# Kernel tuning notes

Measured on AMD Instinct MI355X. Metric: run time of the kernel, lower is better.

The kernel has to match this reference:

```python
import jax, jax.numpy as jnp
import numpy as np

B, S, D, H = 2, 2048, 1024, 16
HD = D // H  # 64

def _make_freqs():
    # flux-style rotation matrices: [1,1,S,HD//2,2,2]
    theta = 10000.0
    inv = 1.0 / (theta ** (np.arange(0, HD, 2, dtype=np.float32) / HD))  # [HD//2]
    pos = np.arange(S, dtype=np.float32)
    ang = pos[:, None] * inv[None, :]  # [S, HD//2]
    cos, sin = np.cos(ang), np.sin(ang)
    rot = np.stack([np.stack([cos, -sin], -1), np.stack([sin, cos], -1)], -2)  # [S,HD//2,2,2]
    return jnp.asarray(rot[None, None], dtype=jnp.float32)

def setup_inputs() -> dict:
    key = jax.random.key(0)
    ks = jax.random.split(key, 9)
    sc = 1.0 / np.sqrt(D)
    return {
        "x": jax.random.normal(ks[0], (B, S, D), jnp.float32),
        "freqs": _make_freqs(),
        "Wq": jax.random.normal(ks[1], (D, D), jnp.float32) * sc,
        "bq": jax.random.normal(ks[2], (D,), jnp.float32) * 0.01,
        "Wk": jax.random.normal(ks[3], (D, D), jnp.float32) * sc,
        "bk": jax.random.normal(ks[4], (D,), jnp.float32) * 0.01,
        "Wv": jax.random.normal(ks[5], (D, D), jnp.float32) * sc,
        "bv": jax.random.normal(ks[6], (D,), jnp.float32) * 0.01,
        "Wo": jax.random.normal(ks[7], (D, D), jnp.float32) * sc,
        "bo": jax.random.normal(ks[8], (D,), jnp.float32) * 0.01,
    }

def _apply_rope(xq, xk, freqs):
    # xq/xk: [B,H,S,HD]; freqs: [1,1,S,HD//2,2,2]
    def rot(t):
        t_ = t.reshape(*t.shape[:-1], -1, 1, 2)  # [B,H,S,HD//2,1,2]
        out = freqs[..., 0] * t_[..., 0] + freqs[..., 1] * t_[..., 1]  # [B,H,S,HD//2,2]
        return out.reshape(t.shape).astype(t.dtype)
    return rot(xq), rot(xk)

def reference(x, freqs, Wq, bq, Wk, bk, Wv, bv, Wo, bo):
    b, s, _ = x.shape
    # QKV projections (torch Linear: x @ W.T + b)
    q = (x @ Wq.T + bq).reshape(b, s, H, HD).transpose(0, 2, 1, 3)  # [B,H,S,HD]
    k = (x @ Wk.T + bk).reshape(b, s, H, HD).transpose(0, 2, 1, 3)
    v = (x @ Wv.T + bv).reshape(b, s, H, HD).transpose(0, 2, 1, 3)
    q, k = _apply_rope(q, k, freqs)
    # scaled dot product attention, no mask, no dropout
    scale = 1.0 / jnp.sqrt(jnp.asarray(HD, x.dtype))
    scores = jnp.einsum("bhqd,bhkd->bhqk", q, k) * scale
    attn = jax.nn.softmax(scores, axis=-1)
    o = jnp.einsum("bhqk,bhkd->bhqd", attn, v)  # [B,H,S,HD]
    o = o.transpose(0, 2, 1, 3).reshape(b, s, D)
    return o @ Wo.T + bo
```

## Files before the change

kernel.cpp:

```cpp
#include <hip/hip_runtime.h>
#include <cmath>

#define B_ 2
#define S_ 2048
#define D_ 1024
#define H_ 16
#define HD_ 64
#define M_ 4096

typedef __attribute__((ext_vector_type(8))) short short8;
typedef __attribute__((ext_vector_type(4))) short short4v;
typedef __attribute__((ext_vector_type(4))) float f32x4;

__device__ __forceinline__ short f2bf(float x) {
    unsigned u = __builtin_bit_cast(unsigned, x);
    u += 0x7fffu + ((u >> 16) & 1u);
    return (short)(u >> 16);
}

__device__ __forceinline__ void gload_lds16(const short* g, short* l) {
    __builtin_amdgcn_global_load_lds(
        (const __attribute__((address_space(1))) unsigned int*)g,
        (__attribute__((address_space(3))) unsigned int*)l, 16, 0, 0);
}

__global__ __launch_bounds__(256) void cast_all_kernel(
    const float* __restrict__ x,  const float* __restrict__ Wq,
    const float* __restrict__ Wk, const float* __restrict__ Wv,
    const float* __restrict__ Wo,
    short* __restrict__ xb, short* __restrict__ Wqkvb, short* __restrict__ Wob)
{
    const size_t i = (size_t)blockIdx.x * 256 + threadIdx.x;
    const float* src; short* dst; size_t off;
    if (i < 1048576)      { src = x;  dst = xb;              off = i; }
    else if (i < 1310720) { src = Wq; dst = Wqkvb;           off = i - 1048576; }
    else if (i < 1572864) { src = Wk; dst = Wqkvb + 1048576; off = i - 1310720; }
    else if (i < 1835008) { src = Wv; dst = Wqkvb + 2097152; off = i - 1572864; }
    else                  { src = Wo; dst = Wob;             off = i - 1835008; }
    float4 v = ((const float4*)src)[off];
    short4v o = { f2bf(v.x), f2bf(v.y), f2bf(v.z), f2bf(v.w) };
    ((short4v*)dst)[off] = o;
}

template<int MODE, int TM, int TN, int NSUB>
__global__ __launch_bounds__(256) void gemm_chunk(
    const short* __restrict__ A, const short* __restrict__ Bw,
    const float* __restrict__ b0p, const float* __restrict__ b1p, const float* __restrict__ b2p,
    const float* __restrict__ freqs,
    void* __restrict__ out0, void* __restrict__ out1, void* __restrict__ out2)
{
    constexpr int RT = TM / 32, CT = TN / 32;
    __shared__ __align__(16) short As[NSUB*TM*32];
    __shared__ __align__(16) short Bs[NSUB*TN*32];
    const int t = threadIdx.x;
    const int w = t >> 6;
    const int lane = t & 63;
    const int qd = lane >> 4, l = lane & 15;
    const int n0 = blockIdx.x * TN, m0 = blockIdx.y * TM;
    const int wr = (w >> 1) * (TM/2), wc = (w & 1) * (TN/2);
    const int srow = lane >> 2;
    const int scol = (lane & 3) * 8;

    f32x4 acc[RT][CT] = {};

    for (int k0 = 0; k0 < 1024; k0 += NSUB*32) {
        __syncthreads();
        #pragma unroll
        for (int sub = 0; sub < NSUB; ++sub) {
            #pragma unroll
            for (int j = 0; j < TM/64; ++j) {
                const int rr = (j*4 + w) * 16;
                gload_lds16(A + (size_t)(m0 + rr + srow)*1024 + k0 + sub*32 + scol,
                            &As[sub*TM*32 + rr*32]);
            }
            #pragma unroll
            for (int j = 0; j < TN/64; ++j) {
                const int rr = (j*4 + w) * 16;
                gload_lds16(Bw + (size_t)(n0 + rr + srow)*1024 + k0 + sub*32 + scol,
                            &Bs[sub*TN*32 + rr*32]);
            }
        }
        __syncthreads();
        #pragma unroll
        for (int sub = 0; sub < NSUB; ++sub) {
            short8 af[RT], bf[CT];
            #pragma unroll
            for (int rt = 0; rt < RT; ++rt)
                af[rt] = *(const short8*)&As[sub*TM*32 + (wr + rt*16 + l)*32 + qd*8];
            #pragma unroll
            for (int ct = 0; ct < CT; ++ct)
                bf[ct] = *(const short8*)&Bs[sub*TN*32 + (wc + ct*16 + l)*32 + qd*8];
            #pragma unroll
            for (int rt = 0; rt < RT; ++rt)
                #pragma unroll
                for (int ct = 0; ct < CT; ++ct)
                    acc[rt][ct] = __builtin_amdgcn_mfma_f32_16x16x32_bf16(af[rt], bf[ct], acc[rt][ct], 0, 0, 0);
        }
    }

    if (MODE == 0) {
        float* out = (float*)out0;
        #pragma unroll
        for (int rt = 0; rt < RT; ++rt)
            #pragma unroll
            for (int ct = 0; ct < CT; ++ct) {
                const int n = n0 + wc + ct*16 + l;
                const float bias = b0p[n];
                #pragma unroll
                for (int r = 0; r < 4; ++r) {
                    const int m = m0 + wr + rt*16 + qd*4 + r;
                    out[(size_t)m*1024 + n] = acc[rt][ct][r] + bias;
                }
            }
    } else {
        const int sel = n0 >> 10;
        const int nb = n0 & 1023;
        const float* bias = (sel == 0) ? b0p : (sel == 1) ? b1p : b2p;
        if (sel < 2) {
            short* outg = (short*)((sel == 0) ? out0 : out1);
            #pragma unroll
            for (int rt = 0; rt < RT; ++rt)
                #pragma unroll
                for (int ct = 0; ct < CT; ++ct) {
                    const int d = nb + wc + ct*16 + l;
                    const float bsv = bias[d];
                    const int h = d >> 6, hd = d & 63;
                    #pragma unroll
                    for (int r = 0; r < 4; ++r) {
                        const int m = m0 + wr + rt*16 + qd*4 + r;
                        const int bb = m >> 11, s = m & 2047;
                        float val = acc[rt][ct][r] + bsv;
                        float pv = __shfl_xor(val, 1);
                        const float* f = freqs + (size_t)s*128 + (size_t)(hd >> 1)*4;
                        float o = (d & 1) ? (f[2]*pv + f[3]*val) : (f[0]*val + f[1]*pv);
                        outg[((size_t)(bb*16 + h)*2048 + s)*64 + hd] = f2bf(o);
                    }
                }
        } else {
            short* outv = (short*)out2;
            #pragma unroll
            for (int rt = 0; rt < RT; ++rt)
                #pragma unroll
                for (int ct = 0; ct < CT; ++ct) {
                    const int d = nb + wc + ct*16 + l;
                    const float bsv = bias[d];
                    const int h = d >> 6, hd = d & 63;
                    const int m0r = m0 + wr + rt*16 + qd*4;
                    const int bb = m0r >> 11, s0 = m0r & 2047;
                    short4v pk;
                    #pragma unroll
                    for (int r = 0; r < 4; ++r) pk[r] = f2bf(acc[rt][ct][r] + bsv);
                    *(short4v*)&outv[((size_t)(bb*16 + h)*64 + hd)*2048 + s0] = pk;
                }
        }
    }
}

__global__ __launch_bounds__(512) void attn_mfma(
    const short* __restrict__ qg, const short* __restrict__ kg,
    const short* __restrict__ vtg, short* __restrict__ og)
{
    __shared__ __align__(16) short Kb[2][64*64];
    __shared__ __align__(16) short Vb[2][64*64];
    __shared__ __align__(16) short Pb[128*64];

    const int t = threadIdx.x;
    const int w = t >> 6;
    const int lane = t & 63;
    const int qd = lane >> 4, l = lane & 15;
    const int l7 = lane & 7;
    const int q0 = blockIdx.x * 128;
    const int bh = blockIdx.y;

    const int rl  = lane >> 3;
    const int ss8 = ((lane & 7) ^ rl) << 3;

    short8 qf[2];
    const short* qb = qg + ((size_t)bh*2048 + q0 + w*16)*64;
    #pragma unroll
    for (int kf = 0; kf < 2; ++kf)
        qf[kf] = *(const short8*)&qb[l*64 + kf*32 + qd*8];

    f32x4 oacc[4] = {};
    float lsum = 0.f;

    const short* kbase = kg  + (size_t)bh*2048*64;
    const short* vbase = vtg + (size_t)bh*64*2048;
    const float SC = 0.125f * 1.44269504088896340736f;

    gload_lds16(kbase + (size_t)(w*8 + rl)*64 + ss8,   &Kb[0][(w*8)*64]);
    gload_lds16(vbase + (size_t)(w*8 + rl)*2048 + ss8, &Vb[0][(w*8)*64]);
    __syncthreads();

    for (int kt = 0; kt < 32; ++kt) {
        const int buf = kt & 1;

        if (kt + 1 < 32) {
            gload_lds16(kbase + (size_t)((kt+1)*64 + w*8 + rl)*64 + ss8,
                        &Kb[buf^1][(w*8)*64]);
            gload_lds16(vbase + (size_t)(w*8 + rl)*2048 + (kt+1)*64 + ss8,
                        &Vb[buf^1][(w*8)*64]);
        }

        f32x4 sacc[4] = {};
        #pragma unroll
        for (int ct = 0; ct < 4; ++ct) {
            short8 k0f = *(const short8*)&Kb[buf][(ct*16 + l)*64 + (((0 + qd) ^ l7) << 3)];
            short8 k1f = *(const short8*)&Kb[buf][(ct*16 + l)*64 + (((4 + qd) ^ l7) << 3)];
            sacc[ct] = __builtin_amdgcn_mfma_f32_16x16x32_bf16(k0f, qf[0], sacc[ct], 0, 0, 0);
            sacc[ct] = __builtin_amdgcn_mfma_f32_16x16x32_bf16(k1f, qf[1], sacc[ct], 0, 0, 0);
        }

        #pragma unroll
        for (int ct = 0; ct < 4; ++ct) {
            float p0 = exp2f(sacc[ct][0] * SC);
            float p1 = exp2f(sacc[ct][1] * SC);
            float p2 = exp2f(sacc[ct][2] * SC);
            float p3 = exp2f(sacc[ct][3] * SC);
            lsum += (p0 + p1) + (p2 + p3);
            union { unsigned u[2]; short4v s; } cv;
            asm("v_cvt_pk_bf16_f32 %0, %1, %2" : "=v"(cv.u[0]) : "v"(p0), "v"(p1));
            asm("v_cvt_pk_bf16_f32 %0, %1, %2" : "=v"(cv.u[1]) : "v"(p2), "v"(p3));
            *(short4v*)&Pb[(w*16 + l)*64 + (((ct*32 + qd*8) ^ (l7 << 4)) >> 1)] = cv.s;
        }

        #pragma unroll
        for (int kf = 0; kf < 2; ++kf) {
            const int so = ((kf*4 + qd) ^ l7) << 3;
            short8 pa = *(const short8*)&Pb[(w*16 + l)*64 + so];
            #pragma unroll
            for (int ht = 0; ht < 4; ++ht) {
                short8 vb = *(const short8*)&Vb[buf][(ht*16 + l)*64 + so];
                oacc[ht] = __builtin_amdgcn_mfma_f32_16x16x32_bf16(pa, vb, oacc[ht], 0, 0, 0);
            }
        }

        __syncthreads();
    }

    lsum += __shfl_xor(lsum, 16);
    lsum += __shfl_xor(lsum, 32);
    float inv[4];
    #pragma unroll
    for (int r = 0; r < 4; ++r)
        inv[r] = 1.0f / __shfl(lsum, qd*4 + r);

    const int bb = bh >> 4, h = bh & 15;
    #pragma unroll
    for (int ht = 0; ht < 4; ++ht)
        #pragma unroll
        for (int r = 0; r < 4; ++r) {
            const int s = q0 + w*16 + qd*4 + r;
            og[((size_t)bb*2048 + s)*1024 + h*64 + ht*16 + l] =
                f2bf(oacc[ht][r] * inv[r]);
        }
}

extern "C" void kernel_launch(void* const* d_in, const int* in_sizes, int n_in,
                              void* d_out, int out_size, void* d_ws, size_t ws_size,
                              hipStream_t stream)
{
    const float* x  = (const float*)d_in[0];
    const float* fr = (const float*)d_in[1];
    const float* Wq = (const float*)d_in[2];
    const float* bq = (const float*)d_in[3];
    const float* Wk = (const float*)d_in[4];
    const float* bk = (const float*)d_in[5];
    const float* Wv = (const float*)d_in[6];
    const float* bv = (const float*)d_in[7];
    const float* Wo = (const float*)d_in[8];
    const float* bo = (const float*)d_in[9];
    float* out = (float*)d_out;

    short* ws    = (short*)d_ws;
    short* xb    = ws;
    short* Wqkvb = xb    + 4194304;
    short* Wob   = Wqkvb + 3145728;
    short* qg    = Wob   + 1048576;
    short* kg    = qg    + 4194304;
    short* vtg   = kg    + 4194304;
    short* og    = vtg   + 4194304;

    cast_all_kernel<<<8192, 256, 0, stream>>>(x, Wq, Wk, Wv, Wo, xb, Wqkvb, Wob);
    gemm_chunk<1,128,128,2><<<dim3(24, 32), 256, 0, stream>>>(xb, Wqkvb, bq, bk, bv, fr, qg, kg, vtg);
    attn_mfma<<<dim3(16, 32), 512, 0, stream>>>(qg, kg, vtg, og);
    gemm_chunk<0,128,64,2><<<dim3(16, 32), 256, 0, stream>>>(og, Wob, bo, nullptr, nullptr, nullptr,
                                                             out, nullptr, nullptr);
}
```

Measured before the change: 253.6 us.

## Double-buffer GEMM LDS tiles with XOR-swizzled layout to overlap loads

```diff
diff --git a/kernel.cpp b/kernel.cpp
--- a/kernel.cpp
+++ b/kernel.cpp
@@ -42,60 +42,78 @@
     ((short4v*)dst)[off] = o;
 }
 
-template<int MODE, int TM, int TN, int NSUB>
-__global__ __launch_bounds__(256) void gemm_chunk(
+template<int MODE, int TM, int TN>
+__global__ __launch_bounds__(256) void gemm_db(
     const short* __restrict__ A, const short* __restrict__ Bw,
     const float* __restrict__ b0p, const float* __restrict__ b1p, const float* __restrict__ b2p,
     const float* __restrict__ freqs,
     void* __restrict__ out0, void* __restrict__ out1, void* __restrict__ out2)
 {
     constexpr int RT = TM / 32, CT = TN / 32;
-    __shared__ __align__(16) short As[NSUB*TM*32];
-    __shared__ __align__(16) short Bs[NSUB*TN*32];
+    __shared__ __align__(16) short Ab[2][TM*64];
+    __shared__ __align__(16) short Bs[2][TN*64];
     const int t = threadIdx.x;
     const int w = t >> 6;
     const int lane = t & 63;
     const int qd = lane >> 4, l = lane & 15;
+    const int l7 = lane & 7;
     const int n0 = blockIdx.x * TN, m0 = blockIdx.y * TM;
     const int wr = (w >> 1) * (TM/2), wc = (w & 1) * (TN/2);
-    const int srow = lane >> 2;
-    const int scol = (lane & 3) * 8;
+    const int rl  = lane >> 3;
+    const int ss8 = ((lane & 7) ^ rl) << 3;
 
     f32x4 acc[RT][CT] = {};
 
-    for (int k0 = 0; k0 < 1024; k0 += NSUB*32) {
-        __syncthreads();
-        #pragma unroll
-        for (int sub = 0; sub < NSUB; ++sub) {
-            #pragma unroll
-            for (int j = 0; j < TM/64; ++j) {
-                const int rr = (j*4 + w) * 16;
-                gload_lds16(A + (size_t)(m0 + rr + srow)*1024 + k0 + sub*32 + scol,
-                            &As[sub*TM*32 + rr*32]);
-            }
-            #pragma unroll
-            for (int j = 0; j < TN/64; ++j) {
-                const int rr = (j*4 + w) * 16;
-                gload_lds16(Bw + (size_t)(n0 + rr + srow)*1024 + k0 + sub*32 + scol,
-                            &Bs[sub*TN*32 + rr*32]);
-            }
-        }
-        __syncthreads();
-        #pragma unroll
-        for (int sub = 0; sub < NSUB; ++sub) {
-            short8 af[RT], bf[CT];
-            #pragma unroll
-            for (int rt = 0; rt < RT; ++rt)
-                af[rt] = *(const short8*)&As[sub*TM*32 + (wr + rt*16 + l)*32 + qd*8];
-            #pragma unroll
-            for (int ct = 0; ct < CT; ++ct)
-                bf[ct] = *(const short8*)&Bs[sub*TN*32 + (wc + ct*16 + l)*32 + qd*8];
+    #pragma unroll
+    for (int j = 0; j < TM/32; ++j) {
+        const int r0 = (j*4 + w) * 8;
+        gload_lds16(A + (size_t)(m0 + r0 + rl)*1024 + ss8, &Ab[0][r0*64]);
+    }
+    #pragma unroll
+    for (int j = 0; j < TN/32; ++j) {
+        const int r0 = (j*4 + w) * 8;
+        gload_lds16(Bw + (size_t)(n0 + r0 + rl)*1024 + ss8, &Bs[0][r0*64]);
+    }
+    __syncthreads();
+
+    for (int kt = 0; kt < 16; ++kt) {
+        const int buf = kt & 1;
+
+        if (kt + 1 < 16) {
+            const int k0 = (kt + 1) * 64;
+            #pragma unroll
+            for (int j = 0; j < TM/32; ++j) {
+                const int r0 = (j*4 + w) * 8;
+                gload_lds16(A + (size_t)(m0 + r0 + rl)*1024 + k0 + ss8, &Ab[buf^1][r0*64]);
+            }
+            #pragma unroll
+            for (int j = 0; j < TN/32; ++j) {
+                const int r0 = (j*4 + w) * 8;
+                gload_lds16(Bw + (size_t)(n0 + r0 + rl)*1024 + k0 + ss8, &Bs[buf^1][r0*64]);
+            }
+        }
+
+        #pragma unroll
+        for (int sub = 0; sub < 2; ++sub) {
+            short8 af[RT], bfr[CT];
+            #pragma unroll
+            for (int rt = 0; rt < RT; ++rt) {
+                const int R = wr + rt*16 + l;
+                af[rt] = *(const short8*)&Ab[buf][R*64 + (((sub*4 + qd) ^ l7) << 3)];
+            }
+            #pragma unroll
+            for (int ct = 0; ct < CT; ++ct) {
+                const int R = wc + ct*16 + l;
+                bfr[ct] = *(const short8*)&Bs[buf][R*64 + (((sub*4 + qd) ^ l7) << 3)];
+            }
             #pragma unroll
             for (int rt = 0; rt < RT; ++rt)
                 #pragma unroll
                 for (int ct = 0; ct < CT; ++ct)
-                    acc[rt][ct] = __builtin_amdgcn_mfma_f32_16x16x32_bf16(af[rt], bf[ct], acc[rt][ct], 0, 0, 0);
-        }
+                    acc[rt][ct] = __builtin_amdgcn_mfma_f32_16x16x32_bf16(af[rt], bfr[ct], acc[rt][ct], 0, 0, 0);
+        }
+
+        __syncthreads();
     }
 
     if (MODE == 0) {
@@ -282,8 +300,8 @@
     short* og    = vtg   + 4194304;
 
     cast_all_kernel<<<8192, 256, 0, stream>>>(x, Wq, Wk, Wv, Wo, xb, Wqkvb, Wob);
-    gemm_chunk<1,128,128,2><<<dim3(24, 32), 256, 0, stream>>>(xb, Wqkvb, bq, bk, bv, fr, qg, kg, vtg);
+    gemm_db<1,128,128><<<dim3(24, 32), 256, 0, stream>>>(xb, Wqkvb, bq, bk, bv, fr, qg, kg, vtg);
     attn_mfma<<<dim3(16, 32), 512, 0, stream>>>(qg, kg, vtg, og);
-    gemm_chunk<0,128,64,2><<<dim3(16, 32), 256, 0, stream>>>(og, Wob, bo, nullptr, nullptr, nullptr,
-                                                             out, nullptr, nullptr);
-}
+    gemm_db<0,128,64><<<dim3(16, 32), 256, 0, stream>>>(og, Wob, bo, nullptr, nullptr, nullptr,
+                                                        out, nullptr, nullptr);
+}
```

Measured after the change: 259.6 us. 1.02x slower.

## Double-buffer GEMM K-loop with swizzled LDS and unroll attention ping-pong

Applied to the files above, without the earlier changes.

```diff
diff --git a/kernel.cpp b/kernel.cpp
--- a/kernel.cpp
+++ b/kernel.cpp
@@ -42,60 +42,68 @@
     ((short4v*)dst)[off] = o;
 }
 
-template<int MODE, int TM, int TN, int NSUB>
-__global__ __launch_bounds__(256) void gemm_chunk(
+template<int MODE, int TM, int TN>
+__global__ __launch_bounds__(256) void gemm_db(
     const short* __restrict__ A, const short* __restrict__ Bw,
     const float* __restrict__ b0p, const float* __restrict__ b1p, const float* __restrict__ b2p,
     const float* __restrict__ freqs,
     void* __restrict__ out0, void* __restrict__ out1, void* __restrict__ out2)
 {
     constexpr int RT = TM / 32, CT = TN / 32;
-    __shared__ __align__(16) short As[NSUB*TM*32];
-    __shared__ __align__(16) short Bs[NSUB*TN*32];
+    __shared__ __align__(16) short A0[TM*32];
+    __shared__ __align__(16) short A1[TM*32];
+    __shared__ __align__(16) short Bs0[TN*32];
+    __shared__ __align__(16) short Bs1[TN*32];
     const int t = threadIdx.x;
     const int w = t >> 6;
     const int lane = t & 63;
     const int qd = lane >> 4, l = lane & 15;
     const int n0 = blockIdx.x * TN, m0 = blockIdx.y * TM;
     const int wr = (w >> 1) * (TM/2), wc = (w & 1) * (TN/2);
-    const int srow = lane >> 2;
-    const int scol = (lane & 3) * 8;
+    const int srow  = lane >> 2;
+    const int sslot = ((lane & 3) ^ ((lane >> 3) & 3)) * 8;
+    const int rsw = (l >> 1) & 3;
 
     f32x4 acc[RT][CT] = {};
 
-    for (int k0 = 0; k0 < 1024; k0 += NSUB*32) {
-        __syncthreads();
-        #pragma unroll
-        for (int sub = 0; sub < NSUB; ++sub) {
-            #pragma unroll
-            for (int j = 0; j < TM/64; ++j) {
-                const int rr = (j*4 + w) * 16;
-                gload_lds16(A + (size_t)(m0 + rr + srow)*1024 + k0 + sub*32 + scol,
-                            &As[sub*TM*32 + rr*32]);
-            }
-            #pragma unroll
-            for (int j = 0; j < TN/64; ++j) {
-                const int rr = (j*4 + w) * 16;
-                gload_lds16(Bw + (size_t)(n0 + rr + srow)*1024 + k0 + sub*32 + scol,
-                            &Bs[sub*TN*32 + rr*32]);
-            }
-        }
-        __syncthreads();
-        #pragma unroll
-        for (int sub = 0; sub < NSUB; ++sub) {
-            short8 af[RT], bf[CT];
-            #pragma unroll
-            for (int rt = 0; rt < RT; ++rt)
-                af[rt] = *(const short8*)&As[sub*TM*32 + (wr + rt*16 + l)*32 + qd*8];
+    auto STAGE = [&](int k0, short* As, short* Bss) {
+        #pragma unroll
+        for (int j = 0; j < TM/64; ++j) {
+            const int r0 = (j*4 + w) * 16;
+            gload_lds16(A + (size_t)(m0 + r0 + srow)*1024 + k0 + sslot, &As[r0*32]);
+        }
+        #pragma unroll
+        for (int j = 0; j < TN/64; ++j) {
+            const int r0 = (j*4 + w) * 16;
+            gload_lds16(Bw + (size_t)(n0 + r0 + srow)*1024 + k0 + sslot, &Bss[r0*32]);
+        }
+    };
+
+    auto COMP = [&](const short* As, const short* Bss) {
+        short8 af[RT], bfr[CT];
+        #pragma unroll
+        for (int rt = 0; rt < RT; ++rt)
+            af[rt] = *(const short8*)&As[(wr + rt*16 + l)*32 + ((qd ^ rsw) << 3)];
+        #pragma unroll
+        for (int ct = 0; ct < CT; ++ct)
+            bfr[ct] = *(const short8*)&Bss[(wc + ct*16 + l)*32 + ((qd ^ rsw) << 3)];
+        #pragma unroll
+        for (int rt = 0; rt < RT; ++rt)
             #pragma unroll
             for (int ct = 0; ct < CT; ++ct)
-                bf[ct] = *(const short8*)&Bs[sub*TN*32 + (wc + ct*16 + l)*32 + qd*8];
-            #pragma unroll
-            for (int rt = 0; rt < RT; ++rt)
-                #pragma unroll
-                for (int ct = 0; ct < CT; ++ct)
-                    acc[rt][ct] = __builtin_amdgcn_mfma_f32_16x16x32_bf16(af[rt], bf[ct], acc[rt][ct], 0, 0, 0);
-        }
+                acc[rt][ct] = __builtin_amdgcn_mfma_f32_16x16x32_bf16(af[rt], bfr[ct], acc[rt][ct], 0, 0, 0);
+    };
+
+    STAGE(0, A0, Bs0);
+    __syncthreads();
+    for (int p = 0; p < 16; ++p) {
+        STAGE((2*p + 1)*32, A1, Bs1);
+        COMP(A0, Bs0);
+        __syncthreads();
+        if (p < 15)
+            STAGE((2*p + 2)*32, A0, Bs0);
+        COMP(A1, Bs1);
+        __syncthreads();
     }
 
     if (MODE == 0) {
@@ -160,8 +168,10 @@
     const short* __restrict__ qg, const short* __restrict__ kg,
     const short* __restrict__ vtg, short* __restrict__ og)
 {
-    __shared__ __align__(16) short Kb[2][64*64];
-    __shared__ __align__(16) short Vb[2][64*64];
+    __shared__ __align__(16) short K0[64*64];
+    __shared__ __align__(16) short K1[64*64];
+    __shared__ __align__(16) short V0[64*64];
+    __shared__ __align__(16) short V1[64*64];
     __shared__ __align__(16) short Pb[128*64];
 
     const int t = threadIdx.x;
@@ -188,29 +198,20 @@
     const short* vbase = vtg + (size_t)bh*64*2048;
     const float SC = 0.125f * 1.44269504088896340736f;
 
-    gload_lds16(kbase + (size_t)(w*8 + rl)*64 + ss8,   &Kb[0][(w*8)*64]);
-    gload_lds16(vbase + (size_t)(w*8 + rl)*2048 + ss8, &Vb[0][(w*8)*64]);
-    __syncthreads();
-
-    for (int kt = 0; kt < 32; ++kt) {
-        const int buf = kt & 1;
-
-        if (kt + 1 < 32) {
-            gload_lds16(kbase + (size_t)((kt+1)*64 + w*8 + rl)*64 + ss8,
-                        &Kb[buf^1][(w*8)*64]);
-            gload_lds16(vbase + (size_t)(w*8 + rl)*2048 + (kt+1)*64 + ss8,
-                        &Vb[buf^1][(w*8)*64]);
-        }
-
+    auto PREF = [&](int c, short* Kd, short* Vd) {
+        gload_lds16(kbase + (size_t)(c*64 + w*8 + rl)*64 + ss8,   &Kd[(w*8)*64]);
+        gload_lds16(vbase + (size_t)(w*8 + rl)*2048 + c*64 + ss8, &Vd[(w*8)*64]);
+    };
+
+    auto TILE = [&](const short* Kc, const short* Vc) {
         f32x4 sacc[4] = {};
         #pragma unroll
         for (int ct = 0; ct < 4; ++ct) {
-            short8 k0f = *(const short8*)&Kb[buf][(ct*16 + l)*64 + (((0 + qd) ^ l7) << 3)];
-            short8 k1f = *(const short8*)&Kb[buf][(ct*16 + l)*64 + (((4 + qd) ^ l7) << 3)];
+            short8 k0f = *(const short8*)&Kc[(ct*16 + l)*64 + (((0 + qd) ^ l7) << 3)];
+            short8 k1f = *(const short8*)&Kc[(ct*16 + l)*64 + (((4 + qd) ^ l7) << 3)];
             sacc[ct] = __builtin_amdgcn_mfma_f32_16x16x32_bf16(k0f, qf[0], sacc[ct], 0, 0, 0);
             sacc[ct] = __builtin_amdgcn_mfma_f32_16x16x32_bf16(k1f, qf[1], sacc[ct], 0, 0, 0);
         }
-
         #pragma unroll
         for (int ct = 0; ct < 4; ++ct) {
             float p0 = exp2f(sacc[ct][0] * SC);
@@ -223,18 +224,27 @@
             asm("v_cvt_pk_bf16_f32 %0, %1, %2" : "=v"(cv.u[1]) : "v"(p2), "v"(p3));
             *(short4v*)&Pb[(w*16 + l)*64 + (((ct*32 + qd*8) ^ (l7 << 4)) >> 1)] = cv.s;
         }
-
         #pragma unroll
         for (int kf = 0; kf < 2; ++kf) {
             const int so = ((kf*4 + qd) ^ l7) << 3;
             short8 pa = *(const short8*)&Pb[(w*16 + l)*64 + so];
             #pragma unroll
             for (int ht = 0; ht < 4; ++ht) {
-                short8 vb = *(const short8*)&Vb[buf][(ht*16 + l)*64 + so];
+                short8 vb = *(const short8*)&Vc[(ht*16 + l)*64 + so];
                 oacc[ht] = __builtin_amdgcn_mfma_f32_16x16x32_bf16(pa, vb, oacc[ht], 0, 0, 0);
             }
         }
-
+    };
+
+    PREF(0, K0, V0);
+    __syncthreads();
+    for (int p = 0; p < 16; ++p) {
+        PREF(2*p + 1, K1, V1);
+        TILE(K0, V0);
+        __syncthreads();
+        if (p < 15)
+            PREF(2*p + 2, K0, V0);
+        TILE(K1, V1);
         __syncthreads();
     }
 
@@ -282,8 +292,8 @@
     short* og    = vtg   + 4194304;
 
     cast_all_kernel<<<8192, 256, 0, stream>>>(x, Wq, Wk, Wv, Wo, xb, Wqkvb, Wob);
-    gemm_chunk<1,128,128,2><<<dim3(24, 32), 256, 0, stream>>>(xb, Wqkvb, bq, bk, bv, fr, qg, kg, vtg);
+    gemm_db<1,128,128><<<dim3(24, 32), 256, 0, stream>>>(xb, Wqkvb, bq, bk, bv, fr, qg, kg, vtg);
     attn_mfma<<<dim3(16, 32), 512, 0, stream>>>(qg, kg, vtg, og);
-    gemm_chunk<0,128,64,2><<<dim3(16, 32), 256, 0, stream>>>(og, Wob, bo, nullptr, nullptr, nullptr,
-                                                             out, nullptr, nullptr);
-}
+    gemm_db<0,64,64><<<dim3(16, 64), 256, 0, stream>>>(og, Wob, bo, nullptr, nullptr, nullptr,
+                                                       out, nullptr, nullptr);
+}
```

New measurement: 247.7 us. 2.3% less time.
